# Kernel tuning notes

Hardware: AMD Instinct MI355X
Metric: run time of the kernel (lower is better)

The kernel has to match this reference:

```python
import jax, jax.numpy as jnp
import numpy as np

B, L, V, E, D, NH, HD, NL = 4, 2048, 32000, 300, 128, 4, 128, 3
D2 = NH * HD  # 512
W = 3  # ring window size (unfold_size)
EPS = 1e-5


def setup_inputs() -> dict:
    key = jax.random.key(0)
    ks = jax.random.split(key, 16)
    s = 0.02
    w = lambda k, shape: (jax.random.normal(k, shape, jnp.float32) * s)
    inp = {
        "tokens": jax.random.randint(ks[0], (B, L), 0, V),
        "mask": jax.random.randint(ks[1], (B, L), 0, 2).astype(jnp.int32),
        "emb_table": w(ks[2], (V, E)),
        "proj_w": w(ks[3], (D, E)),
        "proj_b": jnp.zeros((D,), jnp.float32),
        "ng": jnp.ones((NL, D), jnp.float32),
        "nb": jnp.zeros((NL, D), jnp.float32),
        "rq_w": w(ks[4], (NL, D2, D)), "rq_b": jnp.zeros((NL, D2), jnp.float32),
        "rk_w": w(ks[5], (NL, D2, D)), "rk_b": jnp.zeros((NL, D2), jnp.float32),
        "rv_w": w(ks[6], (NL, D2, D)), "rv_b": jnp.zeros((NL, D2), jnp.float32),
        "ro_w": w(ks[7], (NL, D, D2)), "ro_b": jnp.zeros((NL, D), jnp.float32),
        "sq_w": w(ks[8], (NL, D2, D)), "sq_b": jnp.zeros((NL, D2), jnp.float32),
        "sk_w": w(ks[9], (NL, D2, D)), "sk_b": jnp.zeros((NL, D2), jnp.float32),
        "sv_w": w(ks[10], (NL, D2, D)), "sv_b": jnp.zeros((NL, D2), jnp.float32),
        "so_w": w(ks[11], (NL, D, D2)), "so_b": jnp.zeros((NL, D), jnp.float32),
    }
    return inp


def _layernorm(x, g, b):
    mu = x.mean(-1, keepdims=True)
    var = x.var(-1, keepdims=True)
    return (x - mu) / jnp.sqrt(var + EPS) * g + b


def reference(tokens, mask, emb_table, proj_w, proj_b, ng, nb,
              rq_w, rq_b, rk_w, rk_b, rv_w, rv_b, ro_w, ro_b,
              sq_w, sq_b, sk_w, sk_b, sv_w, sv_b, so_w, so_b):
    b, l = tokens.shape
    pad = (mask == 0)                                        # [B,L] True at padding
    smask = jnp.concatenate([jnp.zeros((b, 1), bool), pad], axis=1)  # [B,L+1]
    x = emb_table[tokens] @ proj_w.T + proj_b                # [B,L,D]
    nodes = x
    relay = x.mean(axis=1)                                   # [B,D]
    r_embs = x                                               # fixed original embeddings
    scale = 1.0 / np.sqrt(HD).astype(np.float32)
    for i in range(NL):
        nx = _layernorm(nodes, ng[i], nb[i])
        # ----- MSA1: ring (windowed) attention + relay extras -----
        q = (nx @ rq_w[i].T + rq_b[i]).reshape(b, l, NH, HD)
        k = (nx @ rk_w[i].T + rk_b[i]).reshape(b, l, NH, HD)
        v = (nx @ rv_w[i].T + rv_b[i]).reshape(b, l, NH, HD)
        relay_bc = jnp.broadcast_to(relay[:, None, :], (b, l, D))
        ax = jnp.stack([r_embs, relay_bc], axis=2)           # [B,L,2,D]
        ak = (ax @ rk_w[i].T + rk_b[i]).reshape(b, l, 2, NH, HD)
        av = (ax @ rv_w[i].T + rv_b[i]).reshape(b, l, 2, NH, HD)
        kp = jnp.pad(k, ((0, 0), (1, 1), (0, 0), (0, 0)))    # zero pad like F.unfold
        vp = jnp.pad(v, ((0, 0), (1, 1), (0, 0), (0, 0)))
        kw = jnp.stack([kp[:, u:u + l] for u in range(W)], axis=2)  # [B,L,3,NH,HD]
        vw = jnp.stack([vp[:, u:u + l] for u in range(W)], axis=2)
        kall = jnp.concatenate([kw, ak], axis=2)             # [B,L,5,NH,HD]
        vall = jnp.concatenate([vw, av], axis=2)
        scores = jnp.einsum('blnh,blunh->blun', q, kall) * scale
        alphas = jax.nn.softmax(scores, axis=2)
        att = jnp.einsum('blun,blunh->blnh', alphas, vall).reshape(b, l, D2)
        nodes = nodes + jax.nn.leaky_relu(att @ ro_w[i].T + ro_b[i])
        # ----- MSA2: relay (global) attention over [relay; nodes] -----
        y = jnp.concatenate([relay[:, None, :], nodes], axis=1)      # [B,L+1,D]
        sq = (relay @ sq_w[i].T + sq_b[i]).reshape(b, NH, HD)
        sk = (y @ sk_w[i].T + sk_b[i]).reshape(b, l + 1, NH, HD)
        sv = (y @ sv_w[i].T + sv_b[i]).reshape(b, l + 1, NH, HD)
        pre = jnp.einsum('bnh,blnh->bnl', sq, sk) * scale            # [B,NH,L+1]
        pre = jnp.where(smask[:, None, :], -jnp.inf, pre)
        al = jax.nn.softmax(pre, axis=2)
        satt = jnp.einsum('bnl,blnh->bnh', al, sv).reshape(b, D2)
        relay = jax.nn.leaky_relu(satt @ so_w[i].T + so_b[i])
        nodes = jnp.where(pad[:, :, None], 0.0, nodes)
    return relay  # a_v: [B, d_model] (use_attention=False path)
```

## Files before the change

kernel.cpp:

```cpp
#include <hip/hip_runtime.h>
#include <hip/hip_bf16.h>

constexpr int B = 4, L = 2048, E = 300, D = 128, NH = 4, HD = 128, NL = 3, D2 = 512;
constexpr float EPS = 1e-5f;
constexpr float SCALE = 0.08838834764831843f;
constexpr int NCH = 64;

typedef unsigned int uint_t;
typedef unsigned short u16;
typedef short bf16x8 __attribute__((ext_vector_type(8)));
typedef float f32x4 __attribute__((ext_vector_type(4)));

__device__ __forceinline__ u16 f2bf(float f) {
  union { float f; uint_t i; } x; x.f = f;
  uint_t r = x.i + 0x7fffu + ((x.i >> 16) & 1u);
  return (u16)(r >> 16);
}
__device__ __forceinline__ uint_t packbf(float a, float b) {
  return (uint_t)f2bf(a) | ((uint_t)f2bf(b) << 16);
}
__device__ __forceinline__ float2 bf2x2(uint_t u) {
  union { uint_t i; float f; } a, b;
  a.i = (u & 0xffffu) << 16; b.i = u & 0xffff0000u;
  return make_float2(a.f, b.f);
}
struct f8 { float v[8]; };
__device__ __forceinline__ f8 unpack8(uint4 u) {
  f8 r;
  float2 a = bf2x2(u.x); r.v[0] = a.x; r.v[1] = a.y;
  float2 b = bf2x2(u.y); r.v[2] = b.x; r.v[3] = b.y;
  float2 c = bf2x2(u.z); r.v[4] = c.x; r.v[5] = c.y;
  float2 d = bf2x2(u.w); r.v[6] = d.x; r.v[7] = d.y;
  return r;
}

struct WCArgs { const float* s[4]; u16* d[4]; };
__global__ __launch_bounds__(256) void wconv(WCArgs wa) {
  int ti = blockIdx.y;
  const float* s = wa.s[ti]; u16* dd = wa.d[ti];
  int i = (blockIdx.x * 256 + threadIdx.x) * 4;
  float4 f = *(const float4*)(s + i);
  *(uint2*)(dd + i) = make_uint2(packbf(f.x, f.y), packbf(f.z, f.w));
}

struct GDesc { const u16* A; const u16* W; const float* bias; u16* outb; };
struct GArgs { GDesc d[5]; };
struct PArgs {
  int mode;
  const float* rel_in;
  const float* pm; const float* ps; const float* pw;
  const float* uprev; const float* cvprev;
  const float* svw; const float* svb;
  const float* sow; const float* sob;
  float* rel_out;
  const float* rkw; const float* rkb;
  const float* rvw; const float* rvb;
  const float* sqw; const float* sqb;
  const float* skw; const float* skb;
  float* relay_k; float* relay_v; float* u; float* cvec;
};

__global__ __launch_bounds__(256) void gemm_qkv(GArgs ga, PArgs pa, int N) {
  __shared__ u16 As[128][136];
  __shared__ u16 Ws[128][136];
  __shared__ float rel[D];
  __shared__ float sql[D2];
  __shared__ float wsum2[NH][D];
  __shared__ float satts[D2];
  __shared__ float ecs2[256];
  int bid = blockIdx.x;
  int t = threadIdx.x;
  if (bid < B) {
    int b = bid;
    int wv = t >> 6, lane = t & 63;
    if (pa.mode) {
      if (t < D) rel[t] = pa.rel_in[(size_t)b * D + t];
      __syncthreads();
      float2 uu = ((const float2*)(pa.uprev + ((size_t)b * NH + wv) * D))[lane];
      float2 rr = ((const float2*)rel)[lane];
      float pdot = uu.x * rr.x + uu.y * rr.y;
#pragma unroll
      for (int o = 1; o < 64; o <<= 1) pdot += __shfl_xor(pdot, o, 64);
      float s0 = pdot + pa.cvprev[b * NH + wv];
      int bn = b * NH + wv;
      float pmv = pa.pm[bn * NCH + lane];
      float m = fmaxf(pmv, s0);
#pragma unroll
      for (int o = 1; o < 64; o <<= 1) m = fmaxf(m, __shfl_xor(m, o, 64));
      float ec = expf(pmv - m);
      ecs2[wv * 64 + lane] = ec;
      float sc = pa.ps[bn * NCH + lane] * ec;
#pragma unroll
      for (int o = 1; o < 64; o <<= 1) sc += __shfl_xor(sc, o, 64);
      float e0 = expf(s0 - m);
      float invS = 1.0f / (e0 + sc);
      float2 a;
      a.x = e0 * rel[lane * 2]; a.y = e0 * rel[lane * 2 + 1];
      const float* pwb = pa.pw + (size_t)bn * NCH * D;
#pragma unroll 8
      for (int c = 0; c < NCH; c++) {
        float2 pw2 = ((const float2*)(pwb + (size_t)c * D))[lane];
        float e = ecs2[wv * 64 + c];
        a.x += e * pw2.x; a.y += e * pw2.y;
      }
      wsum2[wv][lane * 2] = a.x * invS;
      wsum2[wv][lane * 2 + 1] = a.y * invS;
      __syncthreads();
#pragma unroll
      for (int pp = 0; pp < 2; pp++) {
        int nh = pp * 256 + t, n = nh >> 7;
        float acc = pa.svb[nh];
        const float4* wp = (const float4*)(pa.svw + (size_t)nh * D);
        const float4* wl = (const float4*)wsum2[n];
#pragma unroll 8
        for (int dd = 0; dd < D / 4; dd++) {
          float4 x = wl[dd], y = wp[dd];
          acc += x.x * y.x + x.y * y.y + x.z * y.z + x.w * y.w;
        }
        satts[nh] = acc;
      }
      __syncthreads();
      {
        int part = t >> 7, col = t & 127;
        float acc = 0.f;
        const float4* wp = (const float4*)(pa.sow + (size_t)col * D2 + part * 256);
        const float4* a4 = (const float4*)(satts + part * 256);
#pragma unroll 8
        for (int jj = 0; jj < 64; jj++) {
          float4 x = a4[jj], y = wp[jj];
          acc += x.x * y.x + x.y * y.y + x.z * y.z + x.w * y.w;
        }
        ecs2[part * 128 + col] = acc;
      }
      __syncthreads();
      if (t < D) {
        float av = pa.sob[t] + ecs2[t] + ecs2[128 + t];
        av = (av > 0.f) ? av : 0.01f * av;
        rel[t] = av;
        pa.rel_out[(size_t)b * D + t] = av;
      }
      __syncthreads();
    } else {
      if (t < D) rel[t] = pa.rel_in[(size_t)b * D + t];
      __syncthreads();
    }
    const float4* r4 = (const float4*)rel;
#pragma unroll
    for (int pp = 0; pp < 2; pp++) {
      int n = pp * 256 + t;
      float ak_ = pa.rkb[n], av_ = pa.rvb[n], aq_ = pa.sqb[n];
      const float4* wk = (const float4*)(pa.rkw + (size_t)n * D);
      const float4* wv4 = (const float4*)(pa.rvw + (size_t)n * D);
      const float4* wq = (const float4*)(pa.sqw + (size_t)n * D);
#pragma unroll 8
      for (int i2 = 0; i2 < D / 4; i2++) {
        float4 r = r4[i2];
        float4 x = wk[i2]; ak_ += x.x * r.x + x.y * r.y + x.z * r.z + x.w * r.w;
        float4 y = wv4[i2]; av_ += y.x * r.x + y.y * r.y + y.z * r.z + y.w * r.w;
        float4 z = wq[i2]; aq_ += z.x * r.x + z.y * r.y + z.z * r.z + z.w * r.w;
      }
      pa.relay_k[(size_t)b * D2 + n] = ak_;
      pa.relay_v[(size_t)b * D2 + n] = av_;
      sql[n] = aq_;
    }
    __syncthreads();
    {
      float2 sq2 = ((const float2*)(sql + wv * HD))[lane];
      float2 kb2 = ((const float2*)(pa.skb + wv * HD))[lane];
      float cp = sq2.x * kb2.x + sq2.y * kb2.y;
#pragma unroll
      for (int o = 1; o < 64; o <<= 1) cp += __shfl_xor(cp, o, 64);
      if (lane == 0) pa.cvec[b * NH + wv] = cp * SCALE;
    }
#pragma unroll
    for (int pp = 0; pp < 2; pp++) {
      int n = (t >> 7) + 2 * pp, th = t & 127;
      float a0 = 0.f, a1 = 0.f, a2 = 0.f, a3 = 0.f;
      const float* wp = pa.skw + (size_t)(n * HD) * D + th;
      const float* sq = sql + n * HD;
      for (int h = 0; h < HD; h += 4) {
        a0 += sq[h] * wp[(size_t)h * D];
        a1 += sq[h + 1] * wp[(size_t)(h + 1) * D];
        a2 += sq[h + 2] * wp[(size_t)(h + 2) * D];
        a3 += sq[h + 3] * wp[(size_t)(h + 3) * D];
      }
      pa.u[((size_t)b * NH + n) * D + th] = (a0 + a1 + a2 + a3) * SCALE;
    }
    return;
  }
  int g = bid - B;
  int bm = g & 63;
  int y = g >> 6;
  int di = y >> 2, bn = y & 3;
  GDesc d = ga.d[di];
  const int rowA = bm * 128, rowW = bn * 128;

  f32x4 acc[4][4];
#pragma unroll
  for (int i = 0; i < 4; i++)
#pragma unroll
    for (int j = 0; j < 4; j++)
      acc[i][j] = (f32x4){0.f, 0.f, 0.f, 0.f};

  const int r = t >> 1, c0 = (t & 1) * 64;
  const int wid = t >> 6;
  const int wm = (wid & 1) * 64, wn = (wid >> 1) * 64;
  const int lr = t & 15, quad = (t >> 4) & 3;

  const u16* Arow = d.A + (size_t)(rowA + r) * 128;
  const u16* Wrow = d.W + (size_t)(rowW + r) * 128;
  uint4 av_[8], wv_[8];
#pragma unroll
  for (int i = 0; i < 8; i++) {
    av_[i] = *(const uint4*)(Arow + c0 + i * 8);
    wv_[i] = *(const uint4*)(Wrow + c0 + i * 8);
  }
#pragma unroll
  for (int i = 0; i < 8; i++) {
    *(uint4*)&As[r][c0 + i * 8] = av_[i];
    *(uint4*)&Ws[r][c0 + i * 8] = wv_[i];
  }
  __syncthreads();
#pragma unroll
  for (int ks = 0; ks < 4; ks++) {
    bf16x8 af[4], bfr[4];
#pragma unroll
    for (int mt = 0; mt < 4; mt++)
      af[mt] = *(const bf16x8*)&As[wm + mt * 16 + lr][ks * 32 + quad * 8];
#pragma unroll
    for (int nt = 0; nt < 4; nt++)
      bfr[nt] = *(const bf16x8*)&Ws[wn + nt * 16 + lr][ks * 32 + quad * 8];
#pragma unroll
    for (int mt = 0; mt < 4; mt++)
#pragma unroll
      for (int nt = 0; nt < 4; nt++)
        acc[mt][nt] = __builtin_amdgcn_mfma_f32_16x16x32_bf16(af[mt], bfr[nt], acc[mt][nt], 0, 0, 0);
  }
  __syncthreads();
#pragma unroll
  for (int nt = 0; nt < 4; nt++) {
    int colL = wn + nt * 16 + lr;
    float bv = d.bias[rowW + colL];
#pragma unroll
    for (int mt = 0; mt < 4; mt++) {
#pragma unroll
      for (int rr = 0; rr < 4; rr++) {
        int rowL = wm + mt * 16 + quad * 4 + rr;
        As[rowL][colL] = f2bf(acc[mt][nt][rr] + bv);
      }
    }
  }
  __syncthreads();
#pragma unroll
  for (int rep = 0; rep < 8; rep++) {
    int lin = rep * 256 + t;
    int rowL = lin >> 4, colL = (lin & 15) * 8;
    uint4 v = *(const uint4*)&As[rowL][colL];
    *(uint4*)&d.outb[(size_t)(rowA + rowL) * N + rowW + colL] = v;
  }
}

__global__ __launch_bounds__(256) void gemm_embed_ln(
    const float* __restrict__ emb, const float* __restrict__ W,
    const float* __restrict__ bias, const int* __restrict__ gather,
    const float* __restrict__ lng, const float* __restrict__ lnb,
    float* __restrict__ nodes, u16* __restrict__ xb, u16* __restrict__ nxb,
    float* __restrict__ relay) {
  __shared__ u16 As[64][72];
  __shared__ u16 Ws[128][72];
  __shared__ float C[64][132];
  __shared__ float gb[2][D];
  __shared__ float lmu[64], lrs[64];
  int t = threadIdx.x;
  int bm = blockIdx.x;
  const int rowA0 = bm * 64;

  f32x4 acc[2][4];
#pragma unroll
  for (int i = 0; i < 2; i++)
#pragma unroll
    for (int j = 0; j < 4; j++)
      acc[i][j] = (f32x4){0.f, 0.f, 0.f, 0.f};

  const int wid = t >> 6;
  const int wm = (wid & 1) * 32, wn = (wid >> 1) * 64;
  const int lr = t & 15, quad = (t >> 4) & 3;
  const int ra = t >> 2, ca = (t & 3) * 16;
  const int rw = t >> 1, cw = (t & 1) * 32;

  if (t < D) { gb[0][t] = lng[t]; gb[1][t] = lnb[t]; }

  const float* Arow = emb + (size_t)gather[rowA0 + ra] * E;
  const float* Wrow = W + (size_t)rw * E;

  for (int kt = 0; kt < E; kt += 64) {
    __syncthreads();
    bool full = (kt + 64 <= E);
#pragma unroll
    for (int ch = 0; ch < 4; ch++) {
      int c = kt + ca + ch * 4;
      float4 fa;
      if (full) fa = *(const float4*)(Arow + c);
      else {
        fa.x = (c + 0 < E) ? Arow[c + 0] : 0.f;
        fa.y = (c + 1 < E) ? Arow[c + 1] : 0.f;
        fa.z = (c + 2 < E) ? Arow[c + 2] : 0.f;
        fa.w = (c + 3 < E) ? Arow[c + 3] : 0.f;
      }
      *(uint2*)&As[ra][ca + ch * 4] = make_uint2(packbf(fa.x, fa.y), packbf(fa.z, fa.w));
    }
#pragma unroll
    for (int ch = 0; ch < 8; ch++) {
      int c = kt + cw + ch * 4;
      float4 fw;
      if (full) fw = *(const float4*)(Wrow + c);
      else {
        fw.x = (c + 0 < E) ? Wrow[c + 0] : 0.f;
        fw.y = (c + 1 < E) ? Wrow[c + 1] : 0.f;
        fw.z = (c + 2 < E) ? Wrow[c + 2] : 0.f;
        fw.w = (c + 3 < E) ? Wrow[c + 3] : 0.f;
      }
      *(uint2*)&Ws[rw][cw + ch * 4] = make_uint2(packbf(fw.x, fw.y), packbf(fw.z, fw.w));
    }
    __syncthreads();
#pragma unroll
    for (int ks = 0; ks < 2; ks++) {
      bf16x8 af[2], bfr[4];
#pragma unroll
      for (int mt = 0; mt < 2; mt++)
        af[mt] = *(const bf16x8*)&As[wm + mt * 16 + lr][ks * 32 + quad * 8];
#pragma unroll
      for (int nt = 0; nt < 4; nt++)
        bfr[nt] = *(const bf16x8*)&Ws[wn + nt * 16 + lr][ks * 32 + quad * 8];
#pragma unroll
      for (int mt = 0; mt < 2; mt++)
#pragma unroll
        for (int nt = 0; nt < 4; nt++)
          acc[mt][nt] = __builtin_amdgcn_mfma_f32_16x16x32_bf16(af[mt], bfr[nt], acc[mt][nt], 0, 0, 0);
    }
  }
#pragma unroll
  for (int nt = 0; nt < 4; nt++) {
    int col = wn + nt * 16 + lr;
    float bv = bias[col];
#pragma unroll
    for (int mt = 0; mt < 2; mt++) {
#pragma unroll
      for (int rr = 0; rr < 4; rr++) {
        int row = wm + mt * 16 + quad * 4 + rr;
        C[row][col] = acc[mt][nt][rr] + bv;
      }
    }
  }
  __syncthreads();
  if (t < 64) {
    float s = 0.f, s2 = 0.f;
#pragma unroll 16
    for (int j = 0; j < D; j++) { float v = C[t][j]; s += v; s2 += v * v; }
    float mu = s * (1.0f / D);
    float var = s2 * (1.0f / D) - mu * mu;
    lmu[t] = mu; lrs[t] = rsqrtf(var + EPS);
  }
  __syncthreads();
#pragma unroll
  for (int rep = 0; rep < 8; rep++) {
    int lin = rep * 1024 + t * 4;
    int row = lin >> 7, col = lin & 127;
    float4 v = *(const float4*)&C[row][col];
    size_t g = (size_t)(rowA0 + row) * D + col;
    *(float4*)&nodes[g] = v;
    *(uint2*)&xb[g] = make_uint2(packbf(v.x, v.y), packbf(v.z, v.w));
    float mu = lmu[row], rs = lrs[row];
    float o0 = (v.x - mu) * rs * gb[0][col] + gb[1][col];
    float o1 = (v.y - mu) * rs * gb[0][col + 1] + gb[1][col + 1];
    float o2 = (v.z - mu) * rs * gb[0][col + 2] + gb[1][col + 2];
    float o3 = (v.w - mu) * rs * gb[0][col + 3] + gb[1][col + 3];
    *(uint2*)&nxb[g] = make_uint2(packbf(o0, o1), packbf(o2, o3));
  }
  if (t < D) {
    int b = rowA0 >> 11;
    float s = 0.f;
#pragma unroll 16
    for (int r2 = 0; r2 < 64; r2++) s += C[r2][t];
    atomicAdd(&relay[b * D + t], s * (1.0f / L));
  }
}

__global__ __launch_bounds__(512) void attn_ro_ln(
    const u16* __restrict__ q, const u16* __restrict__ k, const u16* __restrict__ v,
    const u16* __restrict__ akr, const u16* __restrict__ avr,
    const float* __restrict__ rkvec, const float* __restrict__ rvvec,
    const u16* __restrict__ W,
    const float* __restrict__ bias,
    const int* __restrict__ mask,
    const float* __restrict__ lng, const float* __restrict__ lnb,
    const float* __restrict__ uvec, const float* __restrict__ cvec,
    float* __restrict__ nodes, u16* __restrict__ nxb,
    float* __restrict__ pm, float* __restrict__ ps, float* __restrict__ pw,
    int do_ln) {
  __shared__ u16 att[32][520];
  __shared__ u16 Ws[128][136];
  __shared__ float C[32][132];
  __shared__ float gb[2][D];
  __shared__ float lmu[32], lrs[32];
  __shared__ float usv[NH][D];
  __shared__ float cv2[NH];
  __shared__ float scs[NH][32];
  __shared__ float esr[NH][32];
  int t = threadIdx.x;
  int bm = blockIdx.x;
  const int rowA0 = bm * 32;
  const int b4 = rowA0 >> 11;
  const int chunk = (rowA0 >> 5) & 63;
  const int wid = t >> 6, lane = t & 63;

  if (do_ln && t < D) { gb[0][t] = lng[t]; gb[1][t] = lnb[t]; }
  usv[t >> 7][t & 127] = uvec[(size_t)b4 * NH * D + t];
  if (t < NH) cv2[t] = cvec[b4 * NH + t];

  {
    size_t rb = (size_t)b4 * D2 + lane * 8;
    float4 rk0 = *(const float4*)(rkvec + rb), rk1 = *(const float4*)(rkvec + rb + 4);
    float4 rv0 = *(const float4*)(rvvec + rb), rv1 = *(const float4*)(rvvec + rb + 4);
    f8 krel, vrel;
    krel.v[0] = rk0.x; krel.v[1] = rk0.y; krel.v[2] = rk0.z; krel.v[3] = rk0.w;
    krel.v[4] = rk1.x; krel.v[5] = rk1.y; krel.v[6] = rk1.z; krel.v[7] = rk1.w;
    vrel.v[0] = rv0.x; vrel.v[1] = rv0.y; vrel.v[2] = rv0.z; vrel.v[3] = rv0.w;
    vrel.v[4] = rv1.x; vrel.v[5] = rv1.y; vrel.v[6] = rv1.z; vrel.v[7] = rv1.w;
#pragma unroll
    for (int i = 0; i < 4; i++) {
      int rr_ = wid * 4 + i;
      int gr = rowA0 + rr_;
      int l = gr & (L - 1);
      size_t rowoff = (size_t)gr * D2 + lane * 8;
      uint4 qd = *(const uint4*)(q + rowoff);
      uint4 kd[4], vd[4];
#pragma unroll
      for (int u2 = 0; u2 < 3; u2++) {
        int ll = l + u2 - 1;
        bool ok = (ll >= 0 && ll < L);
        size_t off = rowoff + (size_t)(u2 - 1) * (size_t)D2;
        if (ok) { kd[u2] = *(const uint4*)(k + off); vd[u2] = *(const uint4*)(v + off); }
        else { kd[u2] = make_uint4(0, 0, 0, 0); vd[u2] = make_uint4(0, 0, 0, 0); }
      }
      kd[3] = *(const uint4*)(akr + rowoff);
      vd[3] = *(const uint4*)(avr + rowoff);
      f8 qf = unpack8(qd);
      f8 kf[5], vf[5];
#pragma unroll
      for (int u2 = 0; u2 < 4; u2++) { kf[u2] = unpack8(kd[u2]); vf[u2] = unpack8(vd[u2]); }
      kf[4] = krel; vf[4] = vrel;
      float s[5];
#pragma unroll
      for (int u2 = 0; u2 < 5; u2++) {
        float p = 0.f;
#pragma unroll
        for (int j = 0; j < 8; j++) p += qf.v[j] * kf[u2].v[j];
#pragma unroll
        for (int o = 1; o < 16; o <<= 1) p += __shfl_xor(p, o, 64);
        s[u2] = p * SCALE;
      }
      float m = s[0];
#pragma unroll
      for (int u2 = 1; u2 < 5; u2++) m = fmaxf(m, s[u2]);
      float e[5], sum = 0.f;
#pragma unroll
      for (int u2 = 0; u2 < 5; u2++) { e[u2] = expf(s[u2] - m); sum += e[u2]; }
      float inv = 1.0f / sum;
      float o8[8];
#pragma unroll
      for (int j = 0; j < 8; j++) {
        float a = 0.f;
#pragma unroll
        for (int u2 = 0; u2 < 5; u2++) a += e[u2] * vf[u2].v[j];
        o8[j] = a * inv;
      }
      uint4 od;
      od.x = packbf(o8[0], o8[1]); od.y = packbf(o8[2], o8[3]);
      od.z = packbf(o8[4], o8[5]); od.w = packbf(o8[6], o8[7]);
      *(uint4*)&att[rr_][lane * 8] = od;
    }
  }
  __syncthreads();

  f32x4 acc[2];
  acc[0] = (f32x4){0.f, 0.f, 0.f, 0.f};
  acc[1] = (f32x4){0.f, 0.f, 0.f, 0.f};
  const int wm = (wid & 1) * 16, wn = (wid >> 1) * 32;
  const int lr = t & 15, quad = (t >> 4) & 3;
  const int rw = t >> 2, cw = (t & 3) * 32;
  const u16* Wrow = W + (size_t)rw * 512;
  for (int kt = 0; kt < 512; kt += 128) {
    uint4 w0 = *(const uint4*)(Wrow + kt + cw);
    uint4 w1 = *(const uint4*)(Wrow + kt + cw + 8);
    uint4 w2 = *(const uint4*)(Wrow + kt + cw + 16);
    uint4 w3 = *(const uint4*)(Wrow + kt + cw + 24);
    __syncthreads();
    *(uint4*)&Ws[rw][cw] = w0; *(uint4*)&Ws[rw][cw + 8] = w1;
    *(uint4*)&Ws[rw][cw + 16] = w2; *(uint4*)&Ws[rw][cw + 24] = w3;
    __syncthreads();
#pragma unroll
    for (int ks = 0; ks < 4; ks++) {
      bf16x8 af = *(const bf16x8*)&att[wm + lr][kt + ks * 32 + quad * 8];
#pragma unroll
      for (int nt = 0; nt < 2; nt++) {
        bf16x8 bfr = *(const bf16x8*)&Ws[wn + nt * 16 + lr][ks * 32 + quad * 8];
        acc[nt] = __builtin_amdgcn_mfma_f32_16x16x32_bf16(af, bfr, acc[nt], 0, 0, 0);
      }
    }
  }
  __syncthreads();
#pragma unroll
  for (int nt = 0; nt < 2; nt++) {
    int col = wn + nt * 16 + lr;
    float bv = bias[col];
#pragma unroll
    for (int rr = 0; rr < 4; rr++) {
      int row = wm + quad * 4 + rr;
      float vv = acc[nt][rr] + bv;
      vv = (vv > 0.f) ? vv : 0.01f * vv;
      vv += nodes[(size_t)(rowA0 + row) * D + col];
      if (mask[rowA0 + row] == 0) vv = 0.f;
      C[row][col] = vv;
    }
  }
  __syncthreads();
  if (t < 32) {
    float s = 0.f, s2 = 0.f;
#pragma unroll 16
    for (int j = 0; j < D; j++) { float vv = C[t][j]; s += vv; s2 += vv * vv; }
    float mu = s * (1.0f / D);
    float var = s2 * (1.0f / D) - mu * mu;
    lmu[t] = mu; lrs[t] = rsqrtf(var + EPS);
  }
  __syncthreads();
#pragma unroll
  for (int rep = 0; rep < 2; rep++) {
    int lin = rep * 2048 + t * 4;
    int row = lin >> 7, col = lin & 127;
    float4 vv = *(const float4*)&C[row][col];
    size_t g = (size_t)(rowA0 + row) * D + col;
    *(float4*)&nodes[g] = vv;
    if (do_ln) {
      float mu = lmu[row], rs = lrs[row];
      float o0 = (vv.x - mu) * rs * gb[0][col] + gb[1][col];
      float o1 = (vv.y - mu) * rs * gb[0][col + 1] + gb[1][col + 1];
      float o2 = (vv.z - mu) * rs * gb[0][col + 2] + gb[1][col + 2];
      float o3 = (vv.w - mu) * rs * gb[0][col + 3] + gb[1][col + 3];
      *(uint2*)&nxb[g] = make_uint2(packbf(o0, o1), packbf(o2, o3));
    }
  }
  if (wid < 4) {
    int n = wid;
    int bn = b4 * NH + n;
    const float2* un = (const float2*)usv[n];
    float2 uv2 = un[lane];
    for (int r2 = 0; r2 < 32; r2++) {
      float2 cc = ((const float2*)&C[r2][0])[lane];
      float p = uv2.x * cc.x + uv2.y * cc.y;
#pragma unroll
      for (int o = 1; o < 64; o <<= 1) p += __shfl_xor(p, o, 64);
      if (lane == 0) {
        float s = p + cv2[n];
        if (mask[rowA0 + r2] == 0) s = -1e30f;
        scs[n][r2] = s;
      }
    }
    float m = -1e30f;
    for (int r2 = 0; r2 < 32; r2++) m = fmaxf(m, scs[n][r2]);
    if (lane < 32) esr[n][lane] = expf(scs[n][lane] - m);
    float sum = 0.f;
    for (int r2 = 0; r2 < 32; r2++) sum += esr[n][r2];
    if (lane == 0) { pm[bn * NCH + chunk] = m; ps[bn * NCH + chunk] = sum; }
    float a0 = 0.f, a1 = 0.f;
    for (int r2 = 0; r2 < 32; r2++) {
      float e = esr[n][r2];
      float2 cc = ((const float2*)&C[r2][0])[lane];
      a0 += e * cc.x; a1 += e * cc.y;
    }
    float* pwp = pw + ((size_t)bn * NCH + chunk) * D + 2 * lane;
    pwp[0] = a0; pwp[1] = a1;
  }
}

__global__ __launch_bounds__(512) void relay_combine(
    const float* __restrict__ pm, const float* __restrict__ ps,
    const float* __restrict__ pw,
    const float* __restrict__ relay_entry,
    const float* __restrict__ uvec_in, const float* __restrict__ cvec_in,
    const float* __restrict__ svw, const float* __restrict__ svb,
    const float* __restrict__ sow, const float* __restrict__ sob,
    float* __restrict__ relay_out) {
  __shared__ float rel0[D];
  __shared__ float wpart[8];
  __shared__ float ecs[NH][NCH];
  __shared__ float wsum[NH][D];
  __shared__ float satts[D2];
  __shared__ float rred[4][D];
  int b = blockIdx.x, t = threadIdx.x;
  int n = t >> 7, h = t & 127;
  int w = t >> 6, lane = t & 63;
  if (t < D) rel0[t] = relay_entry[(size_t)b * D + t];
  __syncthreads();
  float p = uvec_in[((size_t)b * NH + n) * D + h] * rel0[h];
#pragma unroll
  for (int o = 1; o < 64; o <<= 1) p += __shfl_xor(p, o, 64);
  if (lane == 0) wpart[w] = p;
  __syncthreads();
  float s0 = wpart[2 * n] + wpart[2 * n + 1] + cvec_in[b * NH + n];
  int c = h & 63;
  float pmv = pm[(b * NH + n) * NCH + c];
  float m = fmaxf(pmv, s0);
#pragma unroll
  for (int o = 1; o < 64; o <<= 1) m = fmaxf(m, __shfl_xor(m, o, 64));
  float ec = expf(pmv - m);
  if (h < 64) ecs[n][h] = ec;
  float sc = ps[(b * NH + n) * NCH + c] * ec;
#pragma unroll
  for (int o = 1; o < 64; o <<= 1) sc += __shfl_xor(sc, o, 64);
  float e0 = expf(s0 - m);
  float invS = 1.0f / (e0 + sc);
  __syncthreads();
  float acc = e0 * rel0[h];
  const float* pwp = pw + ((size_t)(b * NH + n) * NCH) * D + h;
#pragma unroll 8
  for (int cc = 0; cc < NCH; cc++) acc += ecs[n][cc] * pwp[(size_t)cc * D];
  wsum[n][h] = acc * invS;
  __syncthreads();
  {
    float a = svb[t];
    const float4* wp = (const float4*)(svw + (size_t)t * D);
    const float4* wl = (const float4*)wsum[n];
#pragma unroll 8
    for (int dd = 0; dd < D / 4; dd++) {
      float4 x = wl[dd], y = wp[dd];
      a += x.x * y.x + x.y * y.y + x.z * y.z + x.w * y.w;
    }
    satts[t] = a;
  }
  __syncthreads();
  {
    int part = t >> 7, col = t & 127;
    float a = 0.f;
    const float4* wp = (const float4*)(sow + (size_t)col * D2 + part * 128);
    const float4* a4 = (const float4*)(satts + part * 128);
#pragma unroll 8
    for (int jj = 0; jj < 32; jj++) {
      float4 x = a4[jj], y = wp[jj];
      a += x.x * y.x + x.y * y.y + x.z * y.z + x.w * y.w;
    }
    rred[part][col] = a;
  }
  __syncthreads();
  if (t < D) {
    float a = sob[t] + rred[0][t] + rred[1][t] + rred[2][t] + rred[3][t];
    a = (a > 0.f) ? a : 0.01f * a;
    relay_out[(size_t)b * D + t] = a;
  }
}

extern "C" void kernel_launch(void* const* d_in, const int* in_sizes, int n_in,
                              void* d_out, int out_size, void* d_ws, size_t ws_size,
                              hipStream_t stream) {
  const int* tokens = (const int*)d_in[0];
  const int* mask = (const int*)d_in[1];
  const float* emb = (const float*)d_in[2];
  const float* proj_w = (const float*)d_in[3];
  const float* proj_b = (const float*)d_in[4];
  const float* ng = (const float*)d_in[5];
  const float* nb = (const float*)d_in[6];
  const float* rq_w = (const float*)d_in[7], * rq_b = (const float*)d_in[8];
  const float* rk_w = (const float*)d_in[9], * rk_b = (const float*)d_in[10];
  const float* rv_w = (const float*)d_in[11], * rv_b = (const float*)d_in[12];
  const float* ro_w = (const float*)d_in[13], * ro_b = (const float*)d_in[14];
  const float* sq_w = (const float*)d_in[15], * sq_b = (const float*)d_in[16];
  const float* sk_w = (const float*)d_in[17], * sk_b = (const float*)d_in[18];
  const float* sv_w = (const float*)d_in[19], * sv_b = (const float*)d_in[20];
  const float* so_w = (const float*)d_in[21], * so_b = (const float*)d_in[22];

  const size_t BLD = (size_t)B * L * D;
  const size_t BLD4 = (size_t)B * L * D2;
  const size_t WTEN = (size_t)NL * D * D2;

  float* fp = (float*)d_ws;
  float* nodes = fp;                    fp += BLD;
  float* rbuf0 = fp;                    fp += B * D;
  float* rbuf1 = fp;                    fp += B * D;
  float* relay_k = fp;                  fp += B * D2;
  float* relay_v = fp;                  fp += B * D2;
  float* uv = fp;                       fp += B * NH * D;
  float* cv = fp;                       fp += B * NH;
  float* pm = fp;                       fp += B * NH * NCH;
  float* ps = fp;                       fp += B * NH * NCH;
  float* pw = fp;                       fp += (size_t)B * NH * NCH * D;
  u16* up = (u16*)fp;
  u16* xb = up;                         up += BLD;
  u16* nxb = up;                        up += BLD;
  u16* qb = up;                         up += BLD4;
  u16* kb = up;                         up += BLD4;
  u16* vb = up;                         up += BLD4;
  u16* akb = up;                        up += BLD4;
  u16* avb = up;                        up += BLD4;
  u16* wb = up;
  u16* wrq = wb, * wrk = wb + WTEN, * wrv = wb + 2 * WTEN, * wro = wb + 3 * WTEN;

  hipMemsetAsync(rbuf0, 0, B * D * sizeof(float), stream);

  {
    WCArgs wa;
    wa.s[0] = rq_w; wa.s[1] = rk_w; wa.s[2] = rv_w; wa.s[3] = ro_w;
    wa.d[0] = wrq; wa.d[1] = wrk; wa.d[2] = wrv; wa.d[3] = wro;
    wconv<<<dim3(WTEN / 1024, 4), 256, 0, stream>>>(wa);
  }
  gemm_embed_ln<<<128, 256, 0, stream>>>(emb, proj_w, proj_b, tokens, ng, nb,
                                         nodes, xb, nxb, rbuf0);

  for (int i = 0; i < NL; i++) {
    const size_t wo = (size_t)i * D * D2;
    const float* rqbi = rq_b + (size_t)i * D2;
    const float* rkbi = rk_b + (size_t)i * D2;
    const float* rvbi = rv_b + (size_t)i * D2;
    const float* robi = ro_b + (size_t)i * D;
    const int last = (i == NL - 1);

    {
      GArgs ga = {};
      ga.d[0] = {nxb, wrq + wo, rqbi, qb};
      ga.d[1] = {nxb, wrk + wo, rkbi, kb};
      ga.d[2] = {nxb, wrv + wo, rvbi, vb};
      ga.d[3] = {xb,  wrk + wo, rkbi, akb};
      ga.d[4] = {xb,  wrv + wo, rvbi, avb};
      PArgs pa;
      pa.mode = (i == 0) ? 0 : 1;
      pa.rel_in = (i == 2) ? rbuf1 : rbuf0;
      pa.pm = pm; pa.ps = ps; pa.pw = pw;
      pa.uprev = uv; pa.cvprev = cv;
      const size_t wprev = (size_t)(i > 0 ? i - 1 : 0) * D * D2;
      pa.svw = sv_w + wprev; pa.svb = sv_b + (size_t)(i > 0 ? i - 1 : 0) * D2;
      pa.sow = so_w + wprev; pa.sob = so_b + (size_t)(i > 0 ? i - 1 : 0) * D;
      pa.rel_out = (i == 1) ? rbuf1 : rbuf0;
      pa.rkw = rk_w + wo; pa.rkb = rkbi;
      pa.rvw = rv_w + wo; pa.rvb = rvbi;
      pa.sqw = sq_w + wo; pa.sqb = sq_b + (size_t)i * D2;
      pa.skw = sk_w + wo; pa.skb = sk_b + (size_t)i * D2;
      pa.relay_k = relay_k; pa.relay_v = relay_v; pa.u = uv; pa.cvec = cv;
      gemm_qkv<<<64 * 20 + B, 256, 0, stream>>>(ga, pa, D2);
    }
    attn_ro_ln<<<256, 512, 0, stream>>>(
        qb, kb, vb, akb, avb, relay_k, relay_v,
        wro + wo, robi, mask,
        last ? nullptr : ng + (i + 1) * D, last ? nullptr : nb + (i + 1) * D,
        uv, cv, nodes, nxb, pm, ps, pw, last ? 0 : 1);
  }
  const size_t w2 = (size_t)(NL - 1) * D * D2;
  relay_combine<<<B, 512, 0, stream>>>(pm, ps, pw, rbuf0, uv, cv,
                                       sv_w + w2, sv_b + (size_t)(NL - 1) * D2,
                                       so_w + w2, so_b + (size_t)(NL - 1) * D,
                                       (float*)d_out);
}
```

Baseline: 377.2 us.

## Split per-batch relay projection blocks into six blocks per batch

The relay-side projection work (relay K/V, the relay query, and the u/cvec folding through sk_w) used to run in one block per batch, giving four long serial blocks inside the QKV GEMM launch. It now runs across 24 blocks, six per batch: four compute halves of relay K/V and two compute two heads each of the query plus u/cvec. Because every block now recomputes the previous layer's relay update, u/cvec are double-buffered so readers of the previous values do not race with writers. The cost is redundant recomputation of the relay combine in each of the six blocks and more weight reads.

```diff
diff --git a/kernel.cpp b/kernel.cpp
--- a/kernel.cpp
+++ b/kernel.cpp
@@ -57,21 +57,22 @@
   const float* rvw; const float* rvb;
   const float* sqw; const float* sqb;
   const float* skw; const float* skb;
-  float* relay_k; float* relay_v; float* u; float* cvec;
+  float* relay_k; float* relay_v;
+  float* u; float* cvec;
 };
+constexpr int NPROJ = 24;
 
 __global__ __launch_bounds__(256) void gemm_qkv(GArgs ga, PArgs pa, int N) {
-  __shared__ u16 As[128][136];
-  __shared__ u16 Ws[128][136];
-  __shared__ float rel[D];
-  __shared__ float sql[D2];
-  __shared__ float wsum2[NH][D];
-  __shared__ float satts[D2];
-  __shared__ float ecs2[256];
   int bid = blockIdx.x;
   int t = threadIdx.x;
-  if (bid < B) {
-    int b = bid;
+  if (bid < NPROJ) {
+    __shared__ float rel[D];
+    __shared__ float sql2[2][HD];
+    __shared__ float credp[4];
+    __shared__ float wsum2[NH][D];
+    __shared__ float satts[D2];
+    __shared__ float ecs2[256];
+    int b = bid / 6, j = bid % 6;
     int wv = t >> 6, lane = t & 63;
     if (pa.mode) {
       if (t < D) rel[t] = pa.rel_in[(size_t)b * D + t];
@@ -145,50 +146,52 @@
       __syncthreads();
     }
     const float4* r4 = (const float4*)rel;
-#pragma unroll
-    for (int pp = 0; pp < 2; pp++) {
-      int n = pp * 256 + t;
-      float ak_ = pa.rkb[n], av_ = pa.rvb[n], aq_ = pa.sqb[n];
-      const float4* wk = (const float4*)(pa.rkw + (size_t)n * D);
-      const float4* wv4 = (const float4*)(pa.rvw + (size_t)n * D);
-      const float4* wq = (const float4*)(pa.sqw + (size_t)n * D);
+    if (j < 4) {
+      int which = j >> 1;
+      int n = (j & 1) * 256 + t;
+      const float* W = which ? pa.rvw : pa.rkw;
+      float acc = (which ? pa.rvb : pa.rkb)[n];
+      const float4* w4 = (const float4*)(W + (size_t)n * D);
 #pragma unroll 8
-      for (int i2 = 0; i2 < D / 4; i2++) {
-        float4 r = r4[i2];
-        float4 x = wk[i2]; ak_ += x.x * r.x + x.y * r.y + x.z * r.z + x.w * r.w;
-        float4 y = wv4[i2]; av_ += y.x * r.x + y.y * r.y + y.z * r.z + y.w * r.w;
-        float4 z = wq[i2]; aq_ += z.x * r.x + z.y * r.y + z.z * r.z + z.w * r.w;
-      }
-      pa.relay_k[(size_t)b * D2 + n] = ak_;
-      pa.relay_v[(size_t)b * D2 + n] = av_;
-      sql[n] = aq_;
-    }
-    __syncthreads();
-    {
-      float2 sq2 = ((const float2*)(sql + wv * HD))[lane];
-      float2 kb2 = ((const float2*)(pa.skb + wv * HD))[lane];
-      float cp = sq2.x * kb2.x + sq2.y * kb2.y;
+      for (int i = 0; i < D / 4; i++) {
+        float4 w = w4[i], r = r4[i];
+        acc += w.x * r.x + w.y * r.y + w.z * r.z + w.w * r.w;
+      }
+      (which ? pa.relay_v : pa.relay_k)[(size_t)b * D2 + n] = acc;
+    } else {
+      int hh = t >> 7, th = t & 127;
+      int n = (j - 4) * 2 + hh;
+      int nh = n * HD + th;
+      float acc = pa.sqb[nh];
+      const float4* w4 = (const float4*)(pa.sqw + (size_t)nh * D);
+#pragma unroll 8
+      for (int i = 0; i < D / 4; i++) {
+        float4 w = w4[i], r = r4[i];
+        acc += w.x * r.x + w.y * r.y + w.z * r.z + w.w * r.w;
+      }
+      sql2[hh][th] = acc;
+      __syncthreads();
+      float cp = acc * pa.skb[nh];
 #pragma unroll
       for (int o = 1; o < 64; o <<= 1) cp += __shfl_xor(cp, o, 64);
-      if (lane == 0) pa.cvec[b * NH + wv] = cp * SCALE;
-    }
-#pragma unroll
-    for (int pp = 0; pp < 2; pp++) {
-      int n = (t >> 7) + 2 * pp, th = t & 127;
+      if ((t & 63) == 0) credp[t >> 6] = cp;
       float a0 = 0.f, a1 = 0.f, a2 = 0.f, a3 = 0.f;
       const float* wp = pa.skw + (size_t)(n * HD) * D + th;
-      const float* sq = sql + n * HD;
-      for (int h = 0; h < HD; h += 4) {
-        a0 += sq[h] * wp[(size_t)h * D];
-        a1 += sq[h + 1] * wp[(size_t)(h + 1) * D];
-        a2 += sq[h + 2] * wp[(size_t)(h + 2) * D];
-        a3 += sq[h + 3] * wp[(size_t)(h + 3) * D];
+      for (int hx = 0; hx < HD; hx += 4) {
+        a0 += sql2[hh][hx] * wp[(size_t)hx * D];
+        a1 += sql2[hh][hx + 1] * wp[(size_t)(hx + 1) * D];
+        a2 += sql2[hh][hx + 2] * wp[(size_t)(hx + 2) * D];
+        a3 += sql2[hh][hx + 3] * wp[(size_t)(hx + 3) * D];
       }
       pa.u[((size_t)b * NH + n) * D + th] = (a0 + a1 + a2 + a3) * SCALE;
+      __syncthreads();
+      if (th == 0) pa.cvec[b * NH + n] = (credp[2 * hh] + credp[2 * hh + 1]) * SCALE;
     }
     return;
   }
-  int g = bid - B;
+  __shared__ u16 As[128][136];
+  __shared__ u16 Ws[128][136];
+  int g = bid - NPROJ;
   int bm = g & 63;
   int y = g >> 6;
   int di = y >> 2, bn = y & 3;
@@ -688,8 +691,10 @@
   float* rbuf1 = fp;                    fp += B * D;
   float* relay_k = fp;                  fp += B * D2;
   float* relay_v = fp;                  fp += B * D2;
-  float* uv = fp;                       fp += B * NH * D;
-  float* cv = fp;                       fp += B * NH;
+  float* uv0 = fp;                      fp += B * NH * D;
+  float* uv1 = fp;                      fp += B * NH * D;
+  float* cv0 = fp;                      fp += B * NH;
+  float* cv1 = fp;                      fp += B * NH;
   float* pm = fp;                       fp += B * NH * NCH;
   float* ps = fp;                       fp += B * NH * NCH;
   float* pw = fp;                       fp += (size_t)B * NH * NCH * D;
@@ -704,6 +709,9 @@
   u16* wb = up;
   u16* wrq = wb, * wrk = wb + WTEN, * wrv = wb + 2 * WTEN, * wro = wb + 3 * WTEN;
 
+  float* uv[2] = {uv0, uv1};
+  float* cv[2] = {cv0, cv1};
+
   hipMemsetAsync(rbuf0, 0, B * D * sizeof(float), stream);
 
   {
@@ -714,6 +722,9 @@
   }
   gemm_embed_ln<<<128, 256, 0, stream>>>(emb, proj_w, proj_b, tokens, ng, nb,
                                          nodes, xb, nxb, rbuf0);
+
+  float* rel_in_l[3] = {rbuf0, rbuf0, rbuf1};
+  float* rel_out_l[3] = {nullptr, rbuf1, rbuf0};
 
   for (int i = 0; i < NL; i++) {
     const size_t wo = (size_t)i * D * D2;
@@ -721,6 +732,7 @@
     const float* rkbi = rk_b + (size_t)i * D2;
     const float* rvbi = rv_b + (size_t)i * D2;
     const float* robi = ro_b + (size_t)i * D;
+    const int e = i & 1, ep = (i > 0) ? ((i - 1) & 1) : 0;
     const int last = (i == NL - 1);
 
     {
@@ -732,28 +744,29 @@
       ga.d[4] = {xb,  wrv + wo, rvbi, avb};
       PArgs pa;
       pa.mode = (i == 0) ? 0 : 1;
-      pa.rel_in = (i == 2) ? rbuf1 : rbuf0;
+      pa.rel_in = rel_in_l[i];
       pa.pm = pm; pa.ps = ps; pa.pw = pw;
-      pa.uprev = uv; pa.cvprev = cv;
+      pa.uprev = uv[ep]; pa.cvprev = cv[ep];
       const size_t wprev = (size_t)(i > 0 ? i - 1 : 0) * D * D2;
       pa.svw = sv_w + wprev; pa.svb = sv_b + (size_t)(i > 0 ? i - 1 : 0) * D2;
       pa.sow = so_w + wprev; pa.sob = so_b + (size_t)(i > 0 ? i - 1 : 0) * D;
-      pa.rel_out = (i == 1) ? rbuf1 : rbuf0;
+      pa.rel_out = rel_out_l[i];
       pa.rkw = rk_w + wo; pa.rkb = rkbi;
       pa.rvw = rv_w + wo; pa.rvb = rvbi;
       pa.sqw = sq_w + wo; pa.sqb = sq_b + (size_t)i * D2;
       pa.skw = sk_w + wo; pa.skb = sk_b + (size_t)i * D2;
-      pa.relay_k = relay_k; pa.relay_v = relay_v; pa.u = uv; pa.cvec = cv;
-      gemm_qkv<<<64 * 20 + B, 256, 0, stream>>>(ga, pa, D2);
+      pa.relay_k = relay_k; pa.relay_v = relay_v; pa.u = uv[e]; pa.cvec = cv[e];
+      gemm_qkv<<<64 * 20 + NPROJ, 256, 0, stream>>>(ga, pa, D2);
     }
     attn_ro_ln<<<256, 512, 0, stream>>>(
         qb, kb, vb, akb, avb, relay_k, relay_v,
         wro + wo, robi, mask,
         last ? nullptr : ng + (i + 1) * D, last ? nullptr : nb + (i + 1) * D,
-        uv, cv, nodes, nxb, pm, ps, pw, last ? 0 : 1);
+        uv[e], cv[e], nodes, nxb, pm, ps, pw, last ? 0 : 1);
   }
   const size_t w2 = (size_t)(NL - 1) * D * D2;
-  relay_combine<<<B, 512, 0, stream>>>(pm, ps, pw, rbuf0, uv, cv,
+  relay_combine<<<B, 512, 0, stream>>>(pm, ps, pw, rbuf0,
+                                       uv[(NL - 1) & 1], cv[(NL - 1) & 1],
                                        sv_w + w2, sv_b + (size_t)(NL - 1) * D2,
                                        so_w + w2, so_b + (size_t)(NL - 1) * D,
                                        (float*)d_out);
```

Result: faster. 319.7 us (-15.3%).
